# Kernel tuning notes

Hardware: AMD Instinct MI355X
Metric: run time of the kernel (lower is better)

## Reference

```python
import jax, jax.numpy as jnp
import numpy as np

B, N, D, H = 8, 1024, 1024, 16
HEAD_DIM = D // H
SCALING = HEAD_DIM ** (-0.5)
NEG = -1000000000.0


def setup_inputs() -> dict:
    key = jax.random.key(0)
    ks = jax.random.split(key, 7)
    x = jax.random.normal(ks[0], (B, N, D), dtype=jnp.float32)
    # variable-length batch: lengths in [N//2, N], mask[b, i] = i < len_b
    lengths = jax.random.randint(ks[1], (B,), N // 2, N + 1)
    mask = jnp.arange(N)[None, :] < lengths[:, None]  # [B, N] bool
    s = D ** (-0.5)
    Wk = jax.random.normal(ks[2], (D, D), dtype=jnp.float32) * s
    Wq = jax.random.normal(ks[3], (D, D), dtype=jnp.float32) * s
    Wv = jax.random.normal(ks[4], (D, D), dtype=jnp.float32) * s
    Wo = jax.random.normal(ks[5], (D, D), dtype=jnp.float32) * s
    bo = jnp.zeros((D,), dtype=jnp.float32)
    return {"x": x, "mask": mask, "Wk": Wk, "Wq": Wq, "Wv": Wv, "Wo": Wo, "bo": bo}


def reference(x, mask, Wk, Wq, Wv, Wo, bo):
    # torch nn.Linear: y = x @ W.T
    keys = (x @ Wk.T).reshape(B, N, H, HEAD_DIM)
    queries = (x @ Wq.T).reshape(B, N, H, HEAD_DIM)
    values = (x @ Wv.T).reshape(B, N, H, HEAD_DIM)
    # NOTE: faithful to source: keys on i, queries on j, softmax over j
    scores = jnp.einsum('bihx,bjhx->bhij', keys, queries) * SCALING  # [B,H,N,N]
    pair_mask = mask[:, None, :] & mask[:, :, None]                  # [B,N,N]
    scores = scores + jnp.where(pair_mask, 0.0, NEG)[:, None, :, :]
    attn = jax.nn.softmax(scores, axis=-1)
    out = jnp.einsum('bhij,bjhx->bihx', attn, values)                # [B,N,H,hd]
    out = out.reshape(B, N, D)
    out = out @ Wo.T + bo
    # source does out_dense[mask] (ragged); static-shape equivalent: zero padding
    return out * mask[:, :, None].astype(out.dtype)
```

## Files before the change

kernel.cpp:

```cpp
#include <hip/hip_runtime.h>

typedef unsigned short u16;
typedef __attribute__((ext_vector_type(8))) short short8;
typedef __attribute__((ext_vector_type(4))) short short4v;
typedef __attribute__((ext_vector_type(4))) float f32x4;
typedef __attribute__((ext_vector_type(16))) float f32x16;

#define MFMA16(a, b, c) __builtin_amdgcn_mfma_f32_16x16x32_bf16(a, b, c, 0, 0, 0)
#define MFMA32(a, b, c) __builtin_amdgcn_mfma_f32_32x32x16_bf16(a, b, c, 0, 0, 0)

#define BB 8
#define NN 1024
#define DD 1024
#define HH 16
#define HD 64
#define MM (BB * NN)
#define SCLOG2 0.18033688011112042f

static __device__ __forceinline__ u16 f2bf(float f) {
  unsigned u = __float_as_uint(f);
  u += 0x7fffu + ((u >> 16) & 1u);
  return (u16)(u >> 16);
}

static __device__ __forceinline__ void gld16(const void* g, void* l) {
  __builtin_amdgcn_global_load_lds((const __attribute__((address_space(1))) void*)g,
                                   (__attribute__((address_space(3))) void*)l, 16, 0, 0);
}

static __device__ __forceinline__ unsigned cvtpk(float lo, float hi) {
  unsigned r;
  asm("v_cvt_pk_bf16_f32 %0, %1, %2" : "=v"(r) : "v"(lo), "v"(hi));
  return r;
}

static __device__ __forceinline__ f32x16 zero16() {
  f32x16 v;
#pragma unroll
  for (int i = 0; i < 16; ++i) v[i] = 0.f;
  return v;
}

__global__ void lens_kernel(const unsigned char* __restrict__ mask, int* __restrict__ lens) {
  __shared__ int acc[BB];
  const int t = threadIdx.x;
  if (t < BB) acc[t] = 0;
  __syncthreads();
  const bool isbyte = (mask[1] != 0);
  for (int b = 0; b < BB; ++b) {
    int s = 0;
    if (isbyte) {
      for (int i = t; i < NN; i += 256) s += mask[(size_t)b * NN + i] ? 1 : 0;
    } else {
      const int* mi = (const int*)mask;
      for (int i = t; i < NN; i += 256) s += mi[(size_t)b * NN + i] != 0 ? 1 : 0;
    }
    if (s) atomicAdd(&acc[b], s);
  }
  __syncthreads();
  if (t < BB) lens[t] = acc[t];
}

__global__ __launch_bounds__(256) void cast_bf16_kernel(const float* __restrict__ in,
                                                        u16* __restrict__ out, int n8) {
  const int i = blockIdx.x * 256 + threadIdx.x;
  if (i >= n8) return;
  const f32x4* p = (const f32x4*)in + (size_t)i * 2;
  const f32x4 a = p[0], b = p[1];
  short8 o;
  o[0] = (short)f2bf(a[0]); o[1] = (short)f2bf(a[1]);
  o[2] = (short)f2bf(a[2]); o[3] = (short)f2bf(a[3]);
  o[4] = (short)f2bf(b[0]); o[5] = (short)f2bf(b[1]);
  o[6] = (short)f2bf(b[2]); o[7] = (short)f2bf(b[3]);
  *(short8*)(out + (size_t)i * 8) = o;
}

__global__ __launch_bounds__(256) void cast4_bf16_kernel(const float* __restrict__ a, const float* __restrict__ b,
                                                         const float* __restrict__ c, const float* __restrict__ d,
                                                         u16* __restrict__ oa, u16* __restrict__ ob,
                                                         u16* __restrict__ oc, u16* __restrict__ od) {
  const int i = blockIdx.x * 256 + threadIdx.x;
  const float* in;
  u16* out;
  switch (blockIdx.y) {
    case 0: in = a; out = oa; break;
    case 1: in = b; out = ob; break;
    case 2: in = c; out = oc; break;
    default: in = d; out = od; break;
  }
  const f32x4* p = (const f32x4*)in + (size_t)i * 2;
  const f32x4 va = p[0], vb = p[1];
  short8 o;
  o[0] = (short)f2bf(va[0]); o[1] = (short)f2bf(va[1]);
  o[2] = (short)f2bf(va[2]); o[3] = (short)f2bf(va[3]);
  o[4] = (short)f2bf(vb[0]); o[5] = (short)f2bf(vb[1]);
  o[6] = (short)f2bf(vb[2]); o[7] = (short)f2bf(vb[3]);
  *(short8*)(out + (size_t)i * 8) = o;
}

template <int EPI>
__global__ __launch_bounds__(256) void gemm_bt(const u16* __restrict__ A, const u16* __restrict__ Bw,
                                               void* __restrict__ Cout, const float* __restrict__ bias,
                                               const int* __restrict__ lens, float scale) {
  constexpr int K = 1024;
  __shared__ u16 As[128 * 32];
  __shared__ u16 Bs[128 * 32];
  const int m0 = blockIdx.x * 128;
  const int n0 = blockIdx.y * 128;
  const int t = threadIdx.x;
  const int lane = t & 63;
  const int w = t >> 6;
  const int wr = w >> 1, wc = w & 1;
  const int li = lane & 15, lg = lane >> 4;
  f32x4 acc[4][4] = {};
  const int off0 = t * 16, off1 = (256 + t) * 16;
  const int r0 = off0 >> 6, kb0 = (off0 & 63) >> 1;
  const int r1 = off1 >> 6, kb1 = (off1 & 63) >> 1;

  for (int k0 = 0; k0 < K; k0 += 32) {
    __syncthreads();
    gld16(A + (size_t)(m0 + r0) * K + k0 + kb0, As + off0 / 2);
    gld16(A + (size_t)(m0 + r1) * K + k0 + kb1, As + off1 / 2);
    gld16(Bw + (size_t)(n0 + r0) * K + k0 + kb0, Bs + off0 / 2);
    gld16(Bw + (size_t)(n0 + r1) * K + k0 + kb1, Bs + off1 / 2);
    __syncthreads();
    short8 af[4], bf[4];
#pragma unroll
    for (int mi = 0; mi < 4; ++mi)
      af[mi] = *(const short8*)(As + (wr * 64 + mi * 16 + li) * 32 + lg * 8);
#pragma unroll
    for (int ni = 0; ni < 4; ++ni)
      bf[ni] = *(const short8*)(Bs + (wc * 64 + ni * 16 + li) * 32 + lg * 8);
#pragma unroll
    for (int mi = 0; mi < 4; ++mi)
#pragma unroll
      for (int ni = 0; ni < 4; ++ni) acc[mi][ni] = MFMA16(af[mi], bf[ni], acc[mi][ni]);
  }

  if (EPI == 2) {
    float* C = (float*)Cout;
#pragma unroll
    for (int ni = 0; ni < 4; ++ni) {
      const int col = n0 + wc * 64 + ni * 16 + li;
      const float bv = bias[col];
#pragma unroll
      for (int mi = 0; mi < 4; ++mi) {
        const int rowb = m0 + wr * 64 + mi * 16 + lg * 4;
#pragma unroll
        for (int r = 0; r < 4; ++r) {
          const int row = rowb + r;
          const int bb = row >> 10, ii = row & 1023;
          const float v = (ii < lens[bb]) ? (acc[mi][ni][r] + bv) : 0.f;
          C[(size_t)row * 1024 + col] = v;
        }
      }
    }
  } else if (EPI == 1) {
    u16* Vt = (u16*)Cout;
#pragma unroll
    for (int mi = 0; mi < 4; ++mi) {
      const int row = m0 + wr * 64 + mi * 16 + lg * 4;
      const int bb = row >> 10, jj = row & 1023;
#pragma unroll
      for (int ni = 0; ni < 4; ++ni) {
        const int col = n0 + wc * 64 + ni * 16 + li;
        const int h = col >> 6, x = col & 63;
        short4v st;
#pragma unroll
        for (int r = 0; r < 4; ++r) st[r] = (short)f2bf(acc[mi][ni][r]);
        *(short4v*)(Vt + ((size_t)((bb * HH + h) * HD + x)) * NN + jj) = st;
      }
    }
  } else {
    u16* C = (u16*)Cout;
#pragma unroll
    for (int mi = 0; mi < 4; ++mi)
#pragma unroll
      for (int ni = 0; ni < 4; ++ni) {
        const int col = n0 + wc * 64 + ni * 16 + li;
        const int rowb = m0 + wr * 64 + mi * 16 + lg * 4;
#pragma unroll
        for (int r = 0; r < 4; ++r)
          C[(size_t)(rowb + r) * 1024 + col] = f2bf(acc[mi][ni][r] * scale);
      }
  }
}

__global__ __launch_bounds__(256) void attn_kernel(const u16* __restrict__ Kb, const u16* __restrict__ Qb,
                                                   const u16* __restrict__ Vtb, u16* __restrict__ attb,
                                                   const int* __restrict__ lens) {
  const int ic = blockIdx.x, h = blockIdx.y, b = blockIdx.z;
  const int len = lens[b];
  const int i0 = ic * 128;
  if (i0 >= len) return;
  const int t = threadIdx.x;
  const int w = t >> 6, l = t & 63;
  const int l31 = l & 31, hi = l >> 5;
  const int i0w = i0 + w * 32;

  __shared__ u16 Qs[2][4096];
  __shared__ u16 Vs[2][4096];

  short8 kf[4];
  {
    const u16* kp = Kb + ((size_t)(b * NN + i0w + l31)) * DD + h * HD + hi * 8;
#pragma unroll
    for (int ks = 0; ks < 4; ++ks) kf[ks] = *(const short8*)(kp + ks * 16);
  }

  const size_t qsrc = ((size_t)(b * NN) + l31) * DD + h * HD + w * 16 + hi * 8;
  const size_t vsrc = ((size_t)((b * HH + h) * HD + l31)) * NN + w * 16 + hi * 8;

  auto STAGE = [&](int buf, int j0) {
    u16* qd = &Qs[buf][0] + t * 8;
    u16* vd = &Vs[buf][0] + t * 8;
    gld16(Qb + qsrc + (size_t)j0 * DD, qd);
    gld16(Qb + qsrc + (size_t)(j0 + 32) * DD, qd + 2048);
    gld16(Vtb + vsrc + j0, vd);
    gld16(Vtb + vsrc + 32 * NN + j0, vd + 2048);
  };

  f32x16 o0 = zero16(), o1 = zero16();
  float m_run = -3.0e38f, l_run = 0.f;
  const int nt = (len + 63) >> 6;

  STAGE(0, 0);
  __syncthreads();
  for (int jt = 0; jt < nt; ++jt) {
    const int cur = jt & 1;
    const int j0 = jt * 64;
    if (jt + 1 < nt) STAGE(cur ^ 1, j0 + 64);

    const u16* Qc = &Qs[cur][0];
    const u16* Vc = &Vs[cur][0];
    f32x16 s0 = zero16(), s1 = zero16();
#pragma unroll
    for (int ks = 0; ks < 4; ++ks) {
      const short8 qf = *(const short8*)(Qc + (ks * 64 + l) * 8);
      s0 = MFMA32(qf, kf[ks], s0);
    }
#pragma unroll
    for (int ks = 0; ks < 4; ++ks) {
      const short8 qf = *(const short8*)(Qc + ((4 + ks) * 64 + l) * 8);
      s1 = MFMA32(qf, kf[ks], s1);
    }

    if (j0 + 64 > len) {
#pragma unroll
      for (int r = 0; r < 16; ++r) {
        const int jl = (r & 3) + 8 * (r >> 2) + 4 * hi;
        if (j0 + jl >= len) s0[r] = -3.0e38f;
        if (j0 + 32 + jl >= len) s1[r] = -3.0e38f;
      }
    }

    float pmax = s0[0];
#pragma unroll
    for (int r = 1; r < 16; ++r) pmax = fmaxf(pmax, s0[r]);
#pragma unroll
    for (int r = 0; r < 16; ++r) pmax = fmaxf(pmax, s1[r]);
    pmax = fmaxf(pmax, __shfl_xor(pmax, 32));

    if (!__all(pmax <= m_run + 11.5f)) {
      const float mnew = fmaxf(m_run, pmax);
      const float al = __builtin_amdgcn_exp2f(m_run - mnew);
      l_run *= al;
#pragma unroll
      for (int r = 0; r < 16; ++r) { o0[r] *= al; o1[r] *= al; }
      m_run = mnew;
    }

    float rs = 0.f;
#pragma unroll
    for (int r = 0; r < 16; ++r) { const float p = __builtin_amdgcn_exp2f(s0[r] - m_run); s0[r] = p; rs += p; }
#pragma unroll
    for (int r = 0; r < 16; ++r) { const float p = __builtin_amdgcn_exp2f(s1[r] - m_run); s1[r] = p; rs += p; }
    rs += __shfl_xor(rs, 32);
    l_run += rs;

    short8 pf[4];
#pragma unroll
    for (int jk = 0; jk < 4; ++jk) {
      const f32x16& ss = (jk < 2) ? s0 : s1;
      const int kk = jk & 1;
      unsigned W0 = cvtpk(ss[8 * kk + 0], ss[8 * kk + 1]);
      unsigned W1 = cvtpk(ss[8 * kk + 2], ss[8 * kk + 3]);
      unsigned W2 = cvtpk(ss[8 * kk + 4], ss[8 * kk + 5]);
      unsigned W3 = cvtpk(ss[8 * kk + 6], ss[8 * kk + 7]);
      asm("v_permlane32_swap_b32 %0, %1" : "+v"(W0), "+v"(W2));
      asm("v_permlane32_swap_b32 %0, %1" : "+v"(W1), "+v"(W3));
      union { unsigned u[4]; short8 s; } pu;
      pu.u[0] = W0; pu.u[1] = W1; pu.u[2] = W2; pu.u[3] = W3;
      pf[jk] = pu.s;
    }

#pragma unroll
    for (int kkg = 0; kkg < 4; ++kkg) {
      const short8 vf = *(const short8*)(Vc + (kkg * 64 + l) * 8);
      o0 = MFMA32(vf, pf[kkg], o0);
    }
#pragma unroll
    for (int kkg = 0; kkg < 4; ++kkg) {
      const short8 vf = *(const short8*)(Vc + ((4 + kkg) * 64 + l) * 8);
      o1 = MFMA32(vf, pf[kkg], o1);
    }
    __syncthreads();
  }

  const float inv = 1.f / l_run;
  u16* op = attb + (size_t)(b * NN + i0w + l31) * DD + h * HD + hi * 4;
#pragma unroll
  for (int xs = 0; xs < 2; ++xs) {
    const f32x16& oo = xs ? o1 : o0;
#pragma unroll
    for (int q = 0; q < 4; ++q) {
      short4v st;
#pragma unroll
      for (int e = 0; e < 4; ++e) st[e] = (short)f2bf(oo[q * 4 + e] * inv);
      *(short4v*)(op + xs * 32 + q * 8) = st;
    }
  }
}

extern "C" void kernel_launch(void* const* d_in, const int* in_sizes, int n_in,
                              void* d_out, int out_size, void* d_ws, size_t ws_size,
                              hipStream_t stream) {
  const float* x = (const float*)d_in[0];
  const unsigned char* mask = (const unsigned char*)d_in[1];
  const float* Wk = (const float*)d_in[2];
  const float* Wq = (const float*)d_in[3];
  const float* Wv = (const float*)d_in[4];
  const float* Wo = (const float*)d_in[5];
  const float* bo = (const float*)d_in[6];
  float* out = (float*)d_out;

  char* ws = (char*)d_ws;
  size_t o = 0;
  int* lens = (int*)(ws + o); o += 256;
  u16* xb  = (u16*)(ws + o); o += (size_t)MM * DD * 2;
  u16* wkb = (u16*)(ws + o); o += (size_t)DD * DD * 2;
  u16* wqb = (u16*)(ws + o); o += (size_t)DD * DD * 2;
  u16* wvb = (u16*)(ws + o); o += (size_t)DD * DD * 2;
  u16* wob = (u16*)(ws + o); o += (size_t)DD * DD * 2;
  u16* kb  = (u16*)(ws + o); o += (size_t)MM * DD * 2;
  u16* qb  = (u16*)(ws + o); o += (size_t)MM * DD * 2;
  u16* vtb = (u16*)(ws + o); o += (size_t)MM * DD * 2;
  u16* attb = xb;

  lens_kernel<<<dim3(1), dim3(256), 0, stream>>>(mask, lens);

  const int xn8 = MM * DD / 8;
  cast_bf16_kernel<<<dim3(xn8 / 256), dim3(256), 0, stream>>>(x, xb, xn8);
  cast4_bf16_kernel<<<dim3(DD * DD / 8 / 256, 4), dim3(256), 0, stream>>>(
      Wk, Wq, Wv, Wo, wkb, wqb, wvb, wob);

  const dim3 ggrid(MM / 128, DD / 128);
  gemm_bt<0><<<ggrid, dim3(256), 0, stream>>>(xb, wkb, kb, nullptr, nullptr, SCLOG2);
  gemm_bt<0><<<ggrid, dim3(256), 0, stream>>>(xb, wqb, qb, nullptr, nullptr, 1.0f);
  gemm_bt<1><<<ggrid, dim3(256), 0, stream>>>(xb, wvb, vtb, nullptr, nullptr, 1.0f);

  attn_kernel<<<dim3(NN / 128, HH, BB), dim3(256), 0, stream>>>(kb, qb, vtb, attb, lens);

  gemm_bt<2><<<ggrid, dim3(256), 0, stream>>>(attb, wob, out, bo, lens, 1.0f);
}
```

Baseline: 203.5 us.

## Merge QKV GEMMs into one launch, remap attention blocks, add MFMA priority

Combines the three K/Q/V projection GEMMs into a single launch with a 24-column grid, so one kernel fills the device and per-launch overhead drops. The attention grid becomes a flat 1D launch with a permuted block-to-work mapping that spreads batches and heads across the dispatch order, aiming to balance the variable-length work over CUs/XCDs. It also raises wave priority around the MFMA sections with s_setprio. Early-exit blocks for padded rows now sit interleaved with working blocks, which could change how evenly the load is spread.

```diff
diff --git a/kernel.cpp b/kernel.cpp
--- a/kernel.cpp
+++ b/kernel.cpp
@@ -98,10 +98,82 @@
   *(short8*)(out + (size_t)i * 8) = o;
 }
 
-template <int EPI>
-__global__ __launch_bounds__(256) void gemm_bt(const u16* __restrict__ A, const u16* __restrict__ Bw,
-                                               void* __restrict__ Cout, const float* __restrict__ bias,
-                                               const int* __restrict__ lens, float scale) {
+__global__ __launch_bounds__(256) void gemm_qkv(const u16* __restrict__ A,
+                                                const u16* __restrict__ Wk3, const u16* __restrict__ Wq3,
+                                                const u16* __restrict__ Wv3,
+                                                u16* __restrict__ kb, u16* __restrict__ qb,
+                                                u16* __restrict__ vtb) {
+  constexpr int K = 1024;
+  __shared__ u16 As[128 * 32];
+  __shared__ u16 Bs[128 * 32];
+  const int m0 = blockIdx.x * 128;
+  const int mat = blockIdx.y >> 3;
+  const int n0 = (blockIdx.y & 7) * 128;
+  const u16* Bw = (mat == 0) ? Wk3 : (mat == 1) ? Wq3 : Wv3;
+  const int t = threadIdx.x;
+  const int lane = t & 63;
+  const int w = t >> 6;
+  const int wr = w >> 1, wc = w & 1;
+  const int li = lane & 15, lg = lane >> 4;
+  f32x4 acc[4][4] = {};
+  const int off0 = t * 16, off1 = (256 + t) * 16;
+  const int r0 = off0 >> 6, kb0 = (off0 & 63) >> 1;
+  const int r1 = off1 >> 6, kb1 = (off1 & 63) >> 1;
+
+  for (int k0 = 0; k0 < K; k0 += 32) {
+    __syncthreads();
+    gld16(A + (size_t)(m0 + r0) * K + k0 + kb0, As + off0 / 2);
+    gld16(A + (size_t)(m0 + r1) * K + k0 + kb1, As + off1 / 2);
+    gld16(Bw + (size_t)(n0 + r0) * K + k0 + kb0, Bs + off0 / 2);
+    gld16(Bw + (size_t)(n0 + r1) * K + k0 + kb1, Bs + off1 / 2);
+    __syncthreads();
+    short8 af[4], bf[4];
+#pragma unroll
+    for (int mi = 0; mi < 4; ++mi)
+      af[mi] = *(const short8*)(As + (wr * 64 + mi * 16 + li) * 32 + lg * 8);
+#pragma unroll
+    for (int ni = 0; ni < 4; ++ni)
+      bf[ni] = *(const short8*)(Bs + (wc * 64 + ni * 16 + li) * 32 + lg * 8);
+#pragma unroll
+    for (int mi = 0; mi < 4; ++mi)
+#pragma unroll
+      for (int ni = 0; ni < 4; ++ni) acc[mi][ni] = MFMA16(af[mi], bf[ni], acc[mi][ni]);
+  }
+
+  if (mat == 2) {
+#pragma unroll
+    for (int mi = 0; mi < 4; ++mi) {
+      const int row = m0 + wr * 64 + mi * 16 + lg * 4;
+      const int bb = row >> 10, jj = row & 1023;
+#pragma unroll
+      for (int ni = 0; ni < 4; ++ni) {
+        const int col = n0 + wc * 64 + ni * 16 + li;
+        const int h = col >> 6, x = col & 63;
+        short4v st;
+#pragma unroll
+        for (int r = 0; r < 4; ++r) st[r] = (short)f2bf(acc[mi][ni][r]);
+        *(short4v*)(vtb + ((size_t)((bb * HH + h) * HD + x)) * NN + jj) = st;
+      }
+    }
+  } else {
+    u16* C = (mat == 0) ? kb : qb;
+    const float scale = (mat == 0) ? SCLOG2 : 1.0f;
+#pragma unroll
+    for (int mi = 0; mi < 4; ++mi)
+#pragma unroll
+      for (int ni = 0; ni < 4; ++ni) {
+        const int col = n0 + wc * 64 + ni * 16 + li;
+        const int rowb = m0 + wr * 64 + mi * 16 + lg * 4;
+#pragma unroll
+        for (int r = 0; r < 4; ++r)
+          C[(size_t)(rowb + r) * 1024 + col] = f2bf(acc[mi][ni][r] * scale);
+      }
+  }
+}
+
+__global__ __launch_bounds__(256) void gemm_out(const u16* __restrict__ A, const u16* __restrict__ Bw,
+                                                float* __restrict__ C, const float* __restrict__ bias,
+                                                const int* __restrict__ lens) {
   constexpr int K = 1024;
   __shared__ u16 As[128 * 32];
   __shared__ u16 Bs[128 * 32];
@@ -137,59 +209,30 @@
       for (int ni = 0; ni < 4; ++ni) acc[mi][ni] = MFMA16(af[mi], bf[ni], acc[mi][ni]);
   }
 
-  if (EPI == 2) {
-    float* C = (float*)Cout;
-#pragma unroll
-    for (int ni = 0; ni < 4; ++ni) {
-      const int col = n0 + wc * 64 + ni * 16 + li;
-      const float bv = bias[col];
-#pragma unroll
-      for (int mi = 0; mi < 4; ++mi) {
-        const int rowb = m0 + wr * 64 + mi * 16 + lg * 4;
-#pragma unroll
-        for (int r = 0; r < 4; ++r) {
-          const int row = rowb + r;
-          const int bb = row >> 10, ii = row & 1023;
-          const float v = (ii < lens[bb]) ? (acc[mi][ni][r] + bv) : 0.f;
-          C[(size_t)row * 1024 + col] = v;
-        }
+#pragma unroll
+  for (int ni = 0; ni < 4; ++ni) {
+    const int col = n0 + wc * 64 + ni * 16 + li;
+    const float bv = bias[col];
+#pragma unroll
+    for (int mi = 0; mi < 4; ++mi) {
+      const int rowb = m0 + wr * 64 + mi * 16 + lg * 4;
+#pragma unroll
+      for (int r = 0; r < 4; ++r) {
+        const int row = rowb + r;
+        const int bb = row >> 10, ii = row & 1023;
+        const float v = (ii < lens[bb]) ? (acc[mi][ni][r] + bv) : 0.f;
+        C[(size_t)row * 1024 + col] = v;
       }
     }
-  } else if (EPI == 1) {
-    u16* Vt = (u16*)Cout;
-#pragma unroll
-    for (int mi = 0; mi < 4; ++mi) {
-      const int row = m0 + wr * 64 + mi * 16 + lg * 4;
-      const int bb = row >> 10, jj = row & 1023;
-#pragma unroll
-      for (int ni = 0; ni < 4; ++ni) {
-        const int col = n0 + wc * 64 + ni * 16 + li;
-        const int h = col >> 6, x = col & 63;
-        short4v st;
-#pragma unroll
-        for (int r = 0; r < 4; ++r) st[r] = (short)f2bf(acc[mi][ni][r]);
-        *(short4v*)(Vt + ((size_t)((bb * HH + h) * HD + x)) * NN + jj) = st;
-      }
-    }
-  } else {
-    u16* C = (u16*)Cout;
-#pragma unroll
-    for (int mi = 0; mi < 4; ++mi)
-#pragma unroll
-      for (int ni = 0; ni < 4; ++ni) {
-        const int col = n0 + wc * 64 + ni * 16 + li;
-        const int rowb = m0 + wr * 64 + mi * 16 + lg * 4;
-#pragma unroll
-        for (int r = 0; r < 4; ++r)
-          C[(size_t)(rowb + r) * 1024 + col] = f2bf(acc[mi][ni][r] * scale);
-      }
   }
 }
 
 __global__ __launch_bounds__(256) void attn_kernel(const u16* __restrict__ Kb, const u16* __restrict__ Qb,
                                                    const u16* __restrict__ Vtb, u16* __restrict__ attb,
                                                    const int* __restrict__ lens) {
-  const int ic = blockIdx.x, h = blockIdx.y, b = blockIdx.z;
+  const int bid = blockIdx.x;
+  const int work = (bid & 7) * 128 + (bid >> 3);
+  const int ic = work & 7, h = (work >> 3) & 15, b = work >> 7;
   const int len = lens[b];
   const int i0 = ic * 128;
   if (i0 >= len) return;
@@ -234,6 +277,7 @@
     const u16* Qc = &Qs[cur][0];
     const u16* Vc = &Vs[cur][0];
     f32x16 s0 = zero16(), s1 = zero16();
+    __builtin_amdgcn_s_setprio(1);
 #pragma unroll
     for (int ks = 0; ks < 4; ++ks) {
       const short8 qf = *(const short8*)(Qc + (ks * 64 + l) * 8);
@@ -244,6 +288,7 @@
       const short8 qf = *(const short8*)(Qc + ((4 + ks) * 64 + l) * 8);
       s1 = MFMA32(qf, kf[ks], s1);
     }
+    __builtin_amdgcn_s_setprio(0);
 
     if (j0 + 64 > len) {
 #pragma unroll
@@ -294,6 +339,7 @@
       pf[jk] = pu.s;
     }
 
+    __builtin_amdgcn_s_setprio(1);
 #pragma unroll
     for (int kkg = 0; kkg < 4; ++kkg) {
       const short8 vf = *(const short8*)(Vc + (kkg * 64 + l) * 8);
@@ -304,6 +350,7 @@
       const short8 vf = *(const short8*)(Vc + ((4 + kkg) * 64 + l) * 8);
       o1 = MFMA32(vf, pf[kkg], o1);
     }
+    __builtin_amdgcn_s_setprio(0);
     __syncthreads();
   }
 
@@ -354,12 +401,9 @@
   cast4_bf16_kernel<<<dim3(DD * DD / 8 / 256, 4), dim3(256), 0, stream>>>(
       Wk, Wq, Wv, Wo, wkb, wqb, wvb, wob);
 
-  const dim3 ggrid(MM / 128, DD / 128);
-  gemm_bt<0><<<ggrid, dim3(256), 0, stream>>>(xb, wkb, kb, nullptr, nullptr, SCLOG2);
-  gemm_bt<0><<<ggrid, dim3(256), 0, stream>>>(xb, wqb, qb, nullptr, nullptr, 1.0f);
-  gemm_bt<1><<<ggrid, dim3(256), 0, stream>>>(xb, wvb, vtb, nullptr, nullptr, 1.0f);
-
-  attn_kernel<<<dim3(NN / 128, HH, BB), dim3(256), 0, stream>>>(kb, qb, vtb, attb, lens);
-
-  gemm_bt<2><<<ggrid, dim3(256), 0, stream>>>(attb, wob, out, bo, lens, 1.0f);
-}
+  gemm_qkv<<<dim3(MM / 128, 24), dim3(256), 0, stream>>>(xb, wkb, wqb, wvb, kb, qb, vtb);
+
+  attn_kernel<<<dim3(1024), dim3(256), 0, stream>>>(kb, qb, vtb, attb, lens);
+
+  gemm_out<<<dim3(MM / 128, DD / 128), dim3(256), 0, stream>>>(attb, wob, out, bo, lens);
+}
```

Result: no change. 200.3 us (-1.6%).
